# Kernel tuning notes

Hardware: AMD Instinct MI355X
Metric: run time of the kernel (lower is better)

## Reference

```python
import jax, jax.numpy as jnp
import numpy as np

N_BINS = 15  # module default n_bins


def setup_inputs() -> dict:
    key = jax.random.key(0)
    k1, k2 = jax.random.split(key)
    N, C = 262144, 1000
    logits = jax.random.normal(k1, (N, C), dtype=jnp.float32)
    labels = jax.random.randint(k2, (N,), 0, C)
    return {"logits": logits, "labels": labels}


def reference(logits, labels):
    # softmax over classes, then confidence = max prob, prediction = argmax
    probs = jax.nn.softmax(logits, axis=1)
    confidences = jnp.max(probs, axis=1)          # [N]
    predictions = jnp.argmax(probs, axis=1)       # [N]
    accuracies = (predictions == labels).astype(jnp.float32)

    # bin membership: conf in (i/n_bins, (i+1)/n_bins]  ->  bin i
    # (conf >= 1/C > 0 so the strict lower bound at 0 is never hit)
    bin_ids = jnp.clip(jnp.ceil(confidences * N_BINS).astype(jnp.int32) - 1, 0, N_BINS - 1)

    counts = jax.ops.segment_sum(jnp.ones_like(confidences), bin_ids, num_segments=N_BINS)
    sum_conf = jax.ops.segment_sum(confidences, bin_ids, num_segments=N_BINS)
    sum_acc = jax.ops.segment_sum(accuracies, bin_ids, num_segments=N_BINS)

    n = jnp.float32(confidences.shape[0])
    prop_in_bin = counts / n
    nonempty = counts > 0
    safe_counts = jnp.where(nonempty, counts, 1.0)
    avg_conf = sum_conf / safe_counts
    avg_acc = sum_acc / safe_counts

    ece = jnp.sum(jnp.where(nonempty, jnp.abs(avg_conf - avg_acc) * prop_in_bin, 0.0)).reshape(1)

    # per-bin diagnostics: empty bins report midpoint confidence and 0 accuracy
    boundaries = jnp.linspace(0.0, 1.0, N_BINS + 1)
    midpoints = (boundaries[:-1] + boundaries[1:]) * 0.5
    confs_binned = jnp.where(nonempty, avg_conf, midpoints)
    accs_binned = jnp.where(nonempty, avg_acc, 0.0)

    return ece, confs_binned, accs_binned
```

## Files before the change

kernel.cpp:

```cpp
#include <hip/hip_runtime.h>
#include <math.h>

#define N_BINS 15

__global__ __launch_bounds__(256) void ece_main(const float* __restrict__ logits,
                                                const int* __restrict__ labels,
                                                float* __restrict__ gbins,
                                                int N, int C) {
    __shared__ float sb[3 * N_BINS];
    const int tid = threadIdx.x;
    if (tid < 3 * N_BINS) sb[tid] = 0.0f;
    __syncthreads();

    const int lane = tid & 63;
    const int wid  = tid >> 6;
    const int wavesPerBlock = blockDim.x >> 6;
    const int wavesTotal = gridDim.x * wavesPerBlock;
    const int C4 = C >> 2;

    int row = blockIdx.x * wavesPerBlock + wid;

    float4 v[4];
    if (row < N) {
        const float4* rp = (const float4*)(logits + (size_t)row * C);
        #pragma unroll
        for (int c = 0; c < 4; ++c) {
            int f4i = c * 64 + lane;
            v[c] = (f4i < C4) ? rp[f4i]
                              : make_float4(-INFINITY, -INFINITY, -INFINITY, -INFINITY);
        }
    }

    for (; row < N; row += wavesTotal) {
        int lbl = labels[row];

        int nrow = row + wavesTotal;
        float4 vn[4];
        if (nrow < N) {
            const float4* np = (const float4*)(logits + (size_t)nrow * C);
            #pragma unroll
            for (int c = 0; c < 4; ++c) {
                int f4i = c * 64 + lane;
                vn[c] = (f4i < C4) ? np[f4i]
                                   : make_float4(-INFINITY, -INFINITY, -INFINITY, -INFINITY);
            }
        }

        float m = -INFINITY;
        int   mi = 0x7fffffff;
        #pragma unroll
        for (int c = 0; c < 4; ++c) {
            const float* e = (const float*)&v[c];
            int base = (c * 64 + lane) * 4;
            #pragma unroll
            for (int j = 0; j < 4; ++j) {
                if (e[j] > m) { m = e[j]; mi = base + j; }
            }
        }
        #pragma unroll
        for (int off = 1; off < 64; off <<= 1) {
            float om = __shfl_xor(m, off, 64);
            int   oi = __shfl_xor(mi, off, 64);
            if (om > m || (om == m && oi < mi)) { m = om; mi = oi; }
        }

        float s = 0.0f;
        #pragma unroll
        for (int c = 0; c < 4; ++c) {
            const float* e = (const float*)&v[c];
            #pragma unroll
            for (int j = 0; j < 4; ++j) s += __expf(e[j] - m);
        }
        #pragma unroll
        for (int off = 1; off < 64; off <<= 1) s += __shfl_xor(s, off, 64);

        if (lane == 0) {
            float conf = 1.0f / s;
            int bin = (int)ceilf(conf * (float)N_BINS) - 1;
            bin = bin < 0 ? 0 : (bin > N_BINS - 1 ? N_BINS - 1 : bin);
            float acc = (mi == lbl) ? 1.0f : 0.0f;
            atomicAdd(&sb[bin], 1.0f);
            atomicAdd(&sb[N_BINS + bin], conf);
            atomicAdd(&sb[2 * N_BINS + bin], acc);
        }

        #pragma unroll
        for (int c = 0; c < 4; ++c) v[c] = vn[c];
    }
    __syncthreads();
    if (tid < 3 * N_BINS) atomicAdd(&gbins[tid], sb[tid]);
}

__global__ void ece_final(const float* __restrict__ gbins, float* __restrict__ out,
                          float invN) {
    __shared__ float s_ece[N_BINS];
    int i = threadIdx.x;
    if (i < N_BINS) {
        float cnt   = gbins[i];
        float sconf = gbins[N_BINS + i];
        float sacc  = gbins[2 * N_BINS + i];
        bool  ne    = cnt > 0.0f;
        float sc    = ne ? cnt : 1.0f;
        float avg_conf = sconf / sc;
        float avg_acc  = sacc / sc;
        float prop     = cnt * invN;
        s_ece[i] = ne ? fabsf(avg_conf - avg_acc) * prop : 0.0f;
        out[1 + i]          = ne ? avg_conf : ((float)i + 0.5f) / (float)N_BINS;
        out[1 + N_BINS + i] = ne ? avg_acc  : 0.0f;
    }
    __syncthreads();
    if (i == 0) {
        float e = 0.0f;
        for (int j = 0; j < N_BINS; ++j) e += s_ece[j];
        out[0] = e;
    }
}

extern "C" void kernel_launch(void* const* d_in, const int* in_sizes, int n_in,
                              void* d_out, int out_size, void* d_ws, size_t ws_size,
                              hipStream_t stream) {
    const float* logits = (const float*)d_in[0];
    const int*   labels = (const int*)d_in[1];
    int N = in_sizes[1];
    int C = in_sizes[0] / N;

    float* gbins = (float*)d_ws;
    hipMemsetAsync(gbins, 0, 3 * N_BINS * sizeof(float), stream);

    const int blocks = 2048;
    ece_main<<<blocks, 256, 0, stream>>>(logits, labels, gbins, N, C);
    ece_final<<<1, 64, 0, stream>>>(gbins, (float*)d_out, 1.0f / (float)N);
}
```

Measured before the change: 203.2 us.

## Drop register prefetch and replace global atomics with per-block partials reduction

The main kernel no longer software-prefetches the next row into registers; it loads each row inside the loop, which lowers register pressure. When the workspace is large enough, each block writes its bin sums to its own slot instead of doing global atomics, so the memset is skipped and a 1024-thread final kernel reduces the partials. An atomic fallback is kept for small workspaces. Without the prefetch, load latency is hidden only by occupancy, and the final reduction now reads about 90K partials on a single block.

```diff
diff --git a/kernel.cpp b/kernel.cpp
--- a/kernel.cpp
+++ b/kernel.cpp
@@ -2,14 +2,16 @@
 #include <math.h>
 
 #define N_BINS 15
+#define NSLOTS (3 * N_BINS)
+#define NBLOCKS 2048
 
 __global__ __launch_bounds__(256) void ece_main(const float* __restrict__ logits,
                                                 const int* __restrict__ labels,
-                                                float* __restrict__ gbins,
-                                                int N, int C) {
-    __shared__ float sb[3 * N_BINS];
+                                                float* __restrict__ partial,
+                                                int N, int C, int useAtomic) {
+    __shared__ float sb[NSLOTS];
     const int tid = threadIdx.x;
-    if (tid < 3 * N_BINS) sb[tid] = 0.0f;
+    if (tid < NSLOTS) sb[tid] = 0.0f;
     __syncthreads();
 
     const int lane = tid & 63;
@@ -18,32 +20,15 @@
     const int wavesTotal = gridDim.x * wavesPerBlock;
     const int C4 = C >> 2;
 
-    int row = blockIdx.x * wavesPerBlock + wid;
-
-    float4 v[4];
-    if (row < N) {
+    for (int row = blockIdx.x * wavesPerBlock + wid; row < N; row += wavesTotal) {
+        int lbl = labels[row];
         const float4* rp = (const float4*)(logits + (size_t)row * C);
+        float4 v[4];
         #pragma unroll
         for (int c = 0; c < 4; ++c) {
             int f4i = c * 64 + lane;
             v[c] = (f4i < C4) ? rp[f4i]
                               : make_float4(-INFINITY, -INFINITY, -INFINITY, -INFINITY);
-        }
-    }
-
-    for (; row < N; row += wavesTotal) {
-        int lbl = labels[row];
-
-        int nrow = row + wavesTotal;
-        float4 vn[4];
-        if (nrow < N) {
-            const float4* np = (const float4*)(logits + (size_t)nrow * C);
-            #pragma unroll
-            for (int c = 0; c < 4; ++c) {
-                int f4i = c * 64 + lane;
-                vn[c] = (f4i < C4) ? np[f4i]
-                                   : make_float4(-INFINITY, -INFINITY, -INFINITY, -INFINITY);
-            }
         }
 
         float m = -INFINITY;
@@ -83,33 +68,52 @@
             atomicAdd(&sb[N_BINS + bin], conf);
             atomicAdd(&sb[2 * N_BINS + bin], acc);
         }
-
-        #pragma unroll
-        for (int c = 0; c < 4; ++c) v[c] = vn[c];
     }
     __syncthreads();
-    if (tid < 3 * N_BINS) atomicAdd(&gbins[tid], sb[tid]);
+    if (tid < NSLOTS) {
+        if (useAtomic) atomicAdd(&partial[tid], sb[tid]);
+        else           partial[(size_t)tid * gridDim.x + blockIdx.x] = sb[tid];
+    }
 }
 
-__global__ void ece_final(const float* __restrict__ gbins, float* __restrict__ out,
-                          float invN) {
+__global__ __launch_bounds__(1024) void ece_final(const float* __restrict__ partial,
+                                                  float* __restrict__ out,
+                                                  float invN, int nparts, int useAtomic) {
+    __shared__ float red[NSLOTS];
     __shared__ float s_ece[N_BINS];
-    int i = threadIdx.x;
-    if (i < N_BINS) {
-        float cnt   = gbins[i];
-        float sconf = gbins[N_BINS + i];
-        float sacc  = gbins[2 * N_BINS + i];
+    const int tid = threadIdx.x;
+    const int lane = tid & 63;
+    const int w    = tid >> 6;
+
+    if (useAtomic) {
+        if (tid < NSLOTS) red[tid] = partial[tid];
+    } else {
+        for (int slot = w; slot < NSLOTS; slot += 16) {
+            const float* p = partial + (size_t)slot * nparts;
+            float a = 0.0f;
+            for (int i = lane; i < nparts; i += 64) a += p[i];
+            #pragma unroll
+            for (int off = 1; off < 64; off <<= 1) a += __shfl_xor(a, off, 64);
+            if (lane == 0) red[slot] = a;
+        }
+    }
+    __syncthreads();
+
+    if (tid < N_BINS) {
+        float cnt   = red[tid];
+        float sconf = red[N_BINS + tid];
+        float sacc  = red[2 * N_BINS + tid];
         bool  ne    = cnt > 0.0f;
         float sc    = ne ? cnt : 1.0f;
         float avg_conf = sconf / sc;
         float avg_acc  = sacc / sc;
         float prop     = cnt * invN;
-        s_ece[i] = ne ? fabsf(avg_conf - avg_acc) * prop : 0.0f;
-        out[1 + i]          = ne ? avg_conf : ((float)i + 0.5f) / (float)N_BINS;
-        out[1 + N_BINS + i] = ne ? avg_acc  : 0.0f;
+        s_ece[tid] = ne ? fabsf(avg_conf - avg_acc) * prop : 0.0f;
+        out[1 + tid]          = ne ? avg_conf : ((float)tid + 0.5f) / (float)N_BINS;
+        out[1 + N_BINS + tid] = ne ? avg_acc  : 0.0f;
     }
     __syncthreads();
-    if (i == 0) {
+    if (tid == 0) {
         float e = 0.0f;
         for (int j = 0; j < N_BINS; ++j) e += s_ece[j];
         out[0] = e;
@@ -124,10 +128,14 @@
     int N = in_sizes[1];
     int C = in_sizes[0] / N;
 
-    float* gbins = (float*)d_ws;
-    hipMemsetAsync(gbins, 0, 3 * N_BINS * sizeof(float), stream);
+    float* ws = (float*)d_ws;
+    size_t needed = (size_t)NSLOTS * NBLOCKS * sizeof(float);
+    int useAtomic = (ws_size < needed) ? 1 : 0;
 
-    const int blocks = 2048;
-    ece_main<<<blocks, 256, 0, stream>>>(logits, labels, gbins, N, C);
-    ece_final<<<1, 64, 0, stream>>>(gbins, (float*)d_out, 1.0f / (float)N);
+    if (useAtomic) {
+        hipMemsetAsync(ws, 0, NSLOTS * sizeof(float), stream);
+    }
+    ece_main<<<NBLOCKS, 256, 0, stream>>>(logits, labels, ws, N, C, useAtomic);
+    ece_final<<<1, 1024, 0, stream>>>(ws, (float*)d_out, 1.0f / (float)N,
+                                      NBLOCKS, useAtomic);
 }
```

New measurement: 226.7 us. +11.6%, slower.
